# Kernel optimization log

Hardware: AMD Instinct MI355X
Metric: run time of the kernel (lower is better)

## Reference

```python
import jax, jax.numpy as jnp
import numpy as np

N, E, K, H, F_IN, F_OUT, Q = 50000, 1600000, 4, 4, 32, 32, 1


def setup_inputs() -> dict:
    key = jax.random.key(0)
    ks = jax.random.split(key, 5)
    x = jax.random.normal(ks[0], (N, H, F_IN, Q), dtype=jnp.float32)
    edge_index = jax.random.randint(ks[1], (2, E), 0, N, dtype=jnp.int64)
    edge_weight = jax.random.uniform(ks[2], (E,), dtype=jnp.float32)
    stdv = 1.0 / np.sqrt(F_IN * K)
    weight = jax.random.uniform(ks[3], (K, H, F_IN, F_OUT), dtype=jnp.float32, minval=-stdv, maxval=stdv)
    bias = jax.random.uniform(ks[4], (F_OUT,), dtype=jnp.float32, minval=-stdv, maxval=stdv)
    return {"x": x, "edge_index": edge_index, "edge_weight": edge_weight, "weight": weight, "bias": bias}


def reference(x, edge_index, edge_weight, weight, bias):
    # x: (n, h, f, q); weight: (K, h, f, g); edge_index: (2, E)
    n = x.shape[0]
    row, col = edge_index[0], edge_index[1]
    # remove_self_loops: zero out self-loop edges (static shapes, same math)
    mask = row != col
    ew = jnp.where(mask, edge_weight, jnp.zeros((), x.dtype))
    deg = jax.ops.segment_sum(mask.astype(x.dtype), row, num_segments=n)
    dinv = jnp.where(deg > 0, deg ** -0.5, jnp.zeros((), x.dtype))
    lap = -dinv[row] * ew * dinv[col]  # (E,)

    def spmm(t):
        # out[row] += lap * t[col]; t: (n, h, f, q)
        return jax.ops.segment_sum(lap[:, None, None, None] * t[col], row, num_segments=n)

    Kk = weight.shape[0]
    Tx0 = x
    out = jnp.einsum('nhfq,hfg->ngq', Tx0, weight[0])
    Tx1 = spmm(Tx0)
    out = out + jnp.einsum('nhfq,hfg->ngq', Tx1, weight[1])
    for k in range(2, Kk):
        Tx2 = 2.0 * spmm(Tx1) - Tx0
        out = out + jnp.einsum('nhfq,hfg->ngq', Tx2, weight[k])
        Tx0, Tx1 = Tx1, Tx2
    out = out[:, None]  # (n, 1, g, q) per collapse_H unsqueeze
    out = out + bias.reshape(1, 1, -1, 1)
    return out
```

## Files before the change

### kernel.cpp

```cpp
#include <hip/hip_runtime.h>


#define FEAT 128
#define GOUT 32
#define NCH 4
#define CHF 32
#define SCB 256
#define CH 4096
#define WCAP 16384
#define CAP 12032
#define TROW 160
#define UNR 8

typedef unsigned int uint;
typedef unsigned short ushort;

__device__ __forceinline__ ushort f2bf(float f) {
    uint u = __float_as_uint(f);
    return (ushort)((u + 0x7fffu + ((u >> 16) & 1u)) >> 16);
}
__device__ __forceinline__ float bflo(uint u) { return __uint_as_float(u << 16); }
__device__ __forceinline__ float bfhi(uint u) { return __uint_as_float(u & 0xffff0000u); }
__device__ __forceinline__ int tidx(int i) { return i + ((i >> 4) << 2); }

__global__ __launch_bounds__(1024) void bin_kernel(
    const int* __restrict__ ei, const float* __restrict__ ew, int E,
    int* __restrict__ bucketCursor, uint2* __restrict__ staging) {
    __shared__ int hist[256];
    __shared__ int base[256];
    int e0 = blockIdx.x * CH;
    int e1 = min(e0 + CH, E);
    int t = threadIdx.x;
    if (t < 256) hist[t] = 0;
    __syncthreads();
    for (int e = e0 + t; e < e1; e += 1024) {
        int r = ei[e], c = ei[(size_t)E + e];
        if (r != c) atomicAdd(&hist[r >> 8], 1);
    }
    __syncthreads();
    if (t < 256) {
        int h = hist[t];
        if (h > 0) {
            int run = atomicAdd(&bucketCursor[t], h);
            base[t] = t * CAP + run;
        }
        hist[t] = 0;
    }
    __syncthreads();
    for (int e = e0 + t; e < e1; e += 1024) {
        int r = ei[e], c = ei[(size_t)E + e];
        if (r == c) continue;
        float w = ew[e];
        int bk = r >> 8;
        int j = atomicAdd(&hist[bk], 1);
        int idx = base[bk] + j;
        if (idx < (bk + 1) * CAP)
            staging[idx] = make_uint2(__float_as_uint(w), ((uint)c << 16) | (uint)(r & 255));
    }
}

__global__ __launch_bounds__(256) void bucket_count_kernel(
    const uint2* __restrict__ staging, const int* __restrict__ bucketCursor,
    int* __restrict__ cnt, int n) {
    __shared__ int hist[256];
    int b = blockIdx.x;
    int t = threadIdx.x;
    hist[t] = 0;
    __syncthreads();
    int nrec = bucketCursor[b];
    const uint2* src = staging + (size_t)b * CAP;
    for (int k = t; k < nrec; k += 256)
        atomicAdd(&hist[src[k].y & 255], 1);
    __syncthreads();
    int r = (b << 8) + t;
    if (r < n) cnt[r] = hist[t];
}

__global__ void scan1_kernel(const int* __restrict__ cnt, int* __restrict__ partial,
                             int* __restrict__ blockSums, float* __restrict__ dinv, int n) {
    __shared__ int buf[2][SCB];
    int t = threadIdx.x;
    int i = blockIdx.x * SCB + t;
    int v = (i < n) ? cnt[i] : 0;
    if (i < n) dinv[i] = (v > 0) ? rsqrtf((float)v) : 0.0f;
    buf[0][t] = v;
    __syncthreads();
    int src = 0;
    for (int off = 1; off < SCB; off <<= 1) {
        int d = src ^ 1;
        buf[d][t] = buf[src][t] + ((t >= off) ? buf[src][t - off] : 0);
        __syncthreads();
        src = d;
    }
    int incl = buf[src][t];
    if (i < n) partial[i] = incl - v;
    if (t == SCB - 1) blockSums[blockIdx.x] = incl;
}

__global__ void scan2_kernel(const int* __restrict__ blockSums, int* __restrict__ blockOffsets,
                             int nb, int* __restrict__ total_out) {
    __shared__ int buf[2][SCB];
    __shared__ int carry_s;
    if (threadIdx.x == 0) carry_s = 0;
    __syncthreads();
    for (int base = 0; base < nb; base += SCB) {
        int i = base + (int)threadIdx.x;
        int v = (i < nb) ? blockSums[i] : 0;
        buf[0][threadIdx.x] = v;
        __syncthreads();
        int src = 0;
        for (int off = 1; off < SCB; off <<= 1) {
            int d = src ^ 1;
            buf[d][threadIdx.x] = buf[src][threadIdx.x] +
                                  ((threadIdx.x >= (unsigned)off) ? buf[src][threadIdx.x - off] : 0);
            __syncthreads();
            src = d;
        }
        int incl = buf[src][threadIdx.x];
        int c = carry_s;
        if (i < nb) blockOffsets[i] = c + incl - v;
        __syncthreads();
        if (threadIdx.x == SCB - 1) carry_s = c + incl;
        __syncthreads();
    }
    if (threadIdx.x == 0) *total_out = carry_s;
}

__global__ void scan3_kernel(const int* __restrict__ partial, const int* __restrict__ blockOffsets,
                             int* __restrict__ offsets, int n) {
    int i = blockIdx.x * blockDim.x + threadIdx.x;
    if (i < n) offsets[i] = partial[i] + blockOffsets[i / SCB];
}

__global__ __launch_bounds__(256) void scatter_kernel(
    const uint2* __restrict__ staging, const int* __restrict__ bucketCursor,
    const int* __restrict__ offsets, const float* __restrict__ dinv,
    uint* __restrict__ csr, int n) {
    __shared__ uint win[WCAP];
    __shared__ int roff[256];
    __shared__ int rcur[256];
    __shared__ float dloc[256];
    int b = blockIdx.x;
    int r0 = b << 8;
    int nrows = min(256, n - r0);
    int t = threadIdx.x;
    if (t < nrows) {
        roff[t] = offsets[r0 + t];
        dloc[t] = dinv[r0 + t];
    }
    rcur[t] = 0;
    __syncthreads();
    int wbeg = roff[0];
    int nrec = bucketCursor[b];
    bool fit = (nrec <= WCAP);
    const uint2* src = staging + (size_t)b * CAP;
    for (int k = t; k < nrec; k += 256) {
        uint2 rec = src[k];
        int col = rec.y >> 16;
        int rl = rec.y & 255;
        float lap = -dloc[rl] * __uint_as_float(rec.x) * dinv[col];
        uint colap = ((uint)col << 16) | (uint)f2bf(lap);
        int pos = roff[rl] + atomicAdd(&rcur[rl], 1);
        if (fit) win[pos - wbeg] = colap;
        else csr[pos] = colap;
    }
    __syncthreads();
    if (fit)
        for (int k = t; k < nrec; k += 256) csr[wbeg + k] = win[k];
}

__global__ __launch_bounds__(256) void cvt_einsum0_kernel(
    const float* __restrict__ x, ushort* __restrict__ xb,
    const float* __restrict__ W0, const float* __restrict__ bias,
    float* __restrict__ out, int n) {
    __shared__ __align__(16) float4 sW4[FEAT * GOUT / 4];
    __shared__ __align__(16) float sT[8 * TROW];
    const float* sW = (const float*)sW4;
    int t = threadIdx.x;
    const float4* wsrc = (const float4*)W0;
    for (int idx = t; idx < FEAT * GOUT / 4; idx += 256) sW4[idx] = wsrc[idx];
    int node = blockIdx.x * 8 + (t >> 5);
    int f0 = 4 * (t & 31);
    float4 v = make_float4(0.f, 0.f, 0.f, 0.f);
    if (node < n) {
        v = *(const float4*)(x + (size_t)node * FEAT + f0);
        ushort4 o;
        o.x = f2bf(v.x); o.y = f2bf(v.y); o.z = f2bf(v.z); o.w = f2bf(v.w);
        int j0 = f0 >> 5;
        *(ushort4*)(xb + ((size_t)j0 * n + node) * CHF + (f0 & 31)) = o;
    }
    int nl = t >> 5;
    *(float4*)&sT[nl * TROW + tidx(f0)] = v;
    __syncthreads();
    int l32 = t & 31;
    int q = l32 & 7;
    int part = l32 >> 3;
    float4 a4 = make_float4(0.f, 0.f, 0.f, 0.f);
#pragma unroll
    for (int j = 0; j < 8; ++j) {
        float4 t4 = *(const float4*)&sT[nl * TROW + tidx(part * 32 + 4 * j)];
        const float* wv0 = &sW[(part * 32 + 4 * j) * GOUT + 4 * q];
        float4 w0 = *(const float4*)(wv0);
        float4 w1 = *(const float4*)(wv0 + GOUT);
        float4 w2 = *(const float4*)(wv0 + 2 * GOUT);
        float4 w3 = *(const float4*)(wv0 + 3 * GOUT);
        a4.x += t4.x * w0.x + t4.y * w1.x + t4.z * w2.x + t4.w * w3.x;
        a4.y += t4.x * w0.y + t4.y * w1.y + t4.z * w2.y + t4.w * w3.y;
        a4.z += t4.x * w0.z + t4.y * w1.z + t4.z * w2.z + t4.w * w3.z;
        a4.w += t4.x * w0.w + t4.y * w1.w + t4.z * w2.w + t4.w * w3.w;
    }
    a4.x += __shfl_down(a4.x, 8);  a4.y += __shfl_down(a4.y, 8);
    a4.z += __shfl_down(a4.z, 8);  a4.w += __shfl_down(a4.w, 8);
    a4.x += __shfl_down(a4.x, 16); a4.y += __shfl_down(a4.y, 16);
    a4.z += __shfl_down(a4.z, 16); a4.w += __shfl_down(a4.w, 16);
    if (part == 0 && node < n) {
        const float4 b4 = *(const float4*)(bias + 4 * q);
        float4 r;
        r.x = a4.x + b4.x; r.y = a4.y + b4.y; r.z = a4.z + b4.z; r.w = a4.w + b4.w;
        *(float4*)(out + (size_t)node * GOUT + 4 * q) = r;
    }
}

__global__ __launch_bounds__(512) void spmm_chunk_kernel(
    const ushort* __restrict__ inb, const ushort* __restrict__ sub,
    ushort* __restrict__ outb, const int* __restrict__ offsets,
    const uint* __restrict__ csr, const float* __restrict__ Wk,
    float* __restrict__ out, int n, int has_sub, int nbj) {
    __shared__ __align__(16) float sW[CHF * GOUT];
    __shared__ float sT2[8][8][CHF + 1];
    int j = blockIdx.x / nbj;
    int b = blockIdx.x % nbj;
    int t = threadIdx.x;
    const float4* wsrc = (const float4*)(Wk + j * CHF * GOUT);
    for (int i2 = t; i2 < CHF * GOUT / 4; i2 += 512) ((float4*)sW)[i2] = wsrc[i2];
    int w = t >> 6, lane = t & 63, s = lane >> 3, u = lane & 7;
    int node = b * 64 + w * 8 + s;
    int beg = 0, deg = 0;
    if (node < n) { beg = offsets[node]; deg = offsets[node + 1] - beg; }
    int m = deg;
    m = max(m, __shfl_xor(m, 8));
    m = max(m, __shfl_xor(m, 16));
    m = max(m, __shfl_xor(m, 32));
    const uint2* inb_u2 = (const uint2*)inb;
    size_t jb2 = (size_t)j * n * 8;
    size_t obase = jb2 + (size_t)node * 8 + u;
    uint2 sv = make_uint2(0u, 0u);
    if (has_sub && node < n) sv = ((const uint2*)sub)[obase];
    float a0 = 0.f, a1 = 0.f, a2 = 0.f, a3 = 0.f;
    for (int it = 0; it < m; it += UNR) {
        uint q[UNR];
        uint2 uu[UNR];
#pragma unroll
        for (int k = 0; k < UNR; ++k) {
            int idx = it + k;
            q[k] = (idx < deg) ? csr[beg + idx] : 0u;
        }
#pragma unroll
        for (int k = 0; k < UNR; ++k)
            uu[k] = inb_u2[jb2 + (size_t)(q[k] >> 16) * 8 + u];
#pragma unroll
        for (int k = 0; k < UNR; ++k) {
            float l = bflo(q[k]);
            a0 += l * bflo(uu[k].x);
            a1 += l * bfhi(uu[k].x);
            a2 += l * bflo(uu[k].y);
            a3 += l * bfhi(uu[k].y);
        }
    }
    if (has_sub) {
        a0 = 2.f * a0 - bflo(sv.x);
        a1 = 2.f * a1 - bfhi(sv.x);
        a2 = 2.f * a2 - bflo(sv.y);
        a3 = 2.f * a3 - bfhi(sv.y);
    }
    if (node < n) {
        uint2 o;
        o.x = (uint)f2bf(a0) | ((uint)f2bf(a1) << 16);
        o.y = (uint)f2bf(a2) | ((uint)f2bf(a3) << 16);
        ((uint2*)outb)[obase] = o;
    }
    sT2[w][s][4 * u + 0] = a0;
    sT2[w][s][4 * u + 1] = a1;
    sT2[w][s][4 * u + 2] = a2;
    sT2[w][s][4 * u + 3] = a3;
    __syncthreads();
    float e0 = 0.f, e1 = 0.f, e2 = 0.f, e3 = 0.f;
#pragma unroll
    for (int i = 0; i < CHF; ++i) {
        float tv = sT2[w][s][i];
        e0 += tv * sW[i * GOUT + u];
        e1 += tv * sW[i * GOUT + u + 8];
        e2 += tv * sW[i * GOUT + u + 16];
        e3 += tv * sW[i * GOUT + u + 24];
    }
    if (node < n) {
        float* po = out + (size_t)node * GOUT;
        atomicAdd(po + u, e0);
        atomicAdd(po + u + 8, e1);
        atomicAdd(po + u + 16, e2);
        atomicAdd(po + u + 24, e3);
    }
}

extern "C" void kernel_launch(void* const* d_in, const int* in_sizes, int n_in,
                              void* d_out, int out_size, void* d_ws, size_t ws_size,
                              hipStream_t stream) {
    const float* x = (const float*)d_in[0];
    const int* ei = (const int*)d_in[1];
    const float* ew = (const float*)d_in[2];
    const float* W = (const float*)d_in[3];
    const float* bias = (const float*)d_in[4];
    float* out = (float*)d_out;

    const int N = in_sizes[0] / FEAT;
    const int E = in_sizes[1] / 2;
    const int NB = (N + SCB - 1) / SCB;
    const int NBUK = (N + 255) >> 8;
    const int NBJ = (((N + 63) / 64 + 7) / 8) * 8;

    char* p = (char*)d_ws;
    auto alloc = [&](size_t bytes) {
        char* q = p;
        p += (bytes + 255) & ~(size_t)255;
        return q;
    };
    int* cnt = (int*)alloc((size_t)N * 4);
    int* offsets = (int*)alloc(((size_t)N + 1) * 4);
    float* dinv = (float*)alloc((size_t)N * 4);
    int* partial = (int*)alloc((size_t)N * 4);
    int* blockSums = (int*)alloc((size_t)NB * 4);
    int* blockOffsets = (int*)alloc((size_t)NB * 4);
    int* bucketCursor = (int*)alloc((size_t)NBUK * 4);
    uint* csr = (uint*)alloc(((size_t)E + 64) * 4);
    ushort* xb = (ushort*)alloc((size_t)N * FEAT * 2);
    ushort* Ab = (ushort*)alloc((size_t)N * FEAT * 2);
    ushort* Bb = (ushort*)alloc((size_t)N * FEAT * 2);
    uint2* staging = (uint2*)Ab;
    (void)ws_size;

    hipMemsetAsync(bucketCursor, 0, (size_t)NBUK * 4, stream);

    bin_kernel<<<(E + CH - 1) / CH, 1024, 0, stream>>>(ei, ew, E, bucketCursor, staging);
    bucket_count_kernel<<<NBUK, 256, 0, stream>>>(staging, bucketCursor, cnt, N);
    scan1_kernel<<<NB, SCB, 0, stream>>>(cnt, partial, blockSums, dinv, N);
    scan2_kernel<<<1, SCB, 0, stream>>>(blockSums, blockOffsets, NB, offsets + N);
    scan3_kernel<<<NB, SCB, 0, stream>>>(partial, blockOffsets, offsets, N);
    scatter_kernel<<<NBUK, 256, 0, stream>>>(staging, bucketCursor, offsets, dinv, csr, N);

    cvt_einsum0_kernel<<<(N + 7) / 8, 256, 0, stream>>>(x, xb, W, bias, out, N);

    dim3 sg(NCH * NBJ);
    spmm_chunk_kernel<<<sg, 512, 0, stream>>>(xb, nullptr, Ab, offsets, csr,
                                              W + 1 * FEAT * GOUT, out, N, 0, NBJ);
    spmm_chunk_kernel<<<sg, 512, 0, stream>>>(Ab, xb, Bb, offsets, csr,
                                              W + 2 * FEAT * GOUT, out, N, 1, NBJ);
    spmm_chunk_kernel<<<sg, 512, 0, stream>>>(Bb, Ab, Ab, offsets, csr,
                                              W + 3 * FEAT * GOUT, out, N, 1, NBJ);
}
```

Before: 357.8 us.

## Sort nodes by degree so SpMM waves process similar-length rows

Result: slower. 470.9 us (+31.6%).

```diff
diff --git a/kernel.cpp b/kernel.cpp
--- a/kernel.cpp
+++ b/kernel.cpp
@@ -132,6 +132,45 @@
     if (i < n) offsets[i] = partial[i] + blockOffsets[i / SCB];
 }
 
+__global__ __launch_bounds__(256) void deg_hist_kernel(
+    const int* __restrict__ cnt, int* __restrict__ dhist, int n) {
+    __shared__ int h[256];
+    int t = threadIdx.x;
+    h[t] = 0;
+    __syncthreads();
+    int i = blockIdx.x * 256 + t;
+    if (i < n) atomicAdd(&h[min(cnt[i], 255)], 1);
+    __syncthreads();
+    if (h[t] > 0) atomicAdd(&dhist[t], h[t]);
+}
+
+__global__ __launch_bounds__(256) void deg_scan_kernel(
+    const int* __restrict__ dhist, int* __restrict__ dbase) {
+    __shared__ int buf[2][256];
+    int t = threadIdx.x;
+    int v = dhist[t];
+    buf[0][t] = v;
+    __syncthreads();
+    int src = 0;
+    for (int off = 1; off < 256; off <<= 1) {
+        int d = src ^ 1;
+        buf[d][t] = buf[src][t] + ((t >= off) ? buf[src][t - off] : 0);
+        __syncthreads();
+        src = d;
+    }
+    dbase[t] = buf[src][t] - v;
+}
+
+__global__ __launch_bounds__(256) void deg_scatter_kernel(
+    const int* __restrict__ cnt, const int* __restrict__ dbase,
+    int* __restrict__ dcur, int* __restrict__ perm, int n) {
+    int i = blockIdx.x * 256 + threadIdx.x;
+    if (i >= n) return;
+    int d = min(cnt[i], 255);
+    int pos = dbase[d] + atomicAdd(&dcur[d], 1);
+    perm[pos] = i;
+}
+
 __global__ __launch_bounds__(256) void scatter_kernel(
     const uint2* __restrict__ staging, const int* __restrict__ bucketCursor,
     const int* __restrict__ offsets, const float* __restrict__ dinv,
@@ -224,7 +263,8 @@
 __global__ __launch_bounds__(512) void spmm_chunk_kernel(
     const ushort* __restrict__ inb, const ushort* __restrict__ sub,
     ushort* __restrict__ outb, const int* __restrict__ offsets,
-    const uint* __restrict__ csr, const float* __restrict__ Wk,
+    const uint* __restrict__ csr, const int* __restrict__ perm,
+    const float* __restrict__ Wk,
     float* __restrict__ out, int n, int has_sub, int nbj) {
     __shared__ __align__(16) float sW[CHF * GOUT];
     __shared__ float sT2[8][8][CHF + 1];
@@ -234,7 +274,8 @@
     const float4* wsrc = (const float4*)(Wk + j * CHF * GOUT);
     for (int i2 = t; i2 < CHF * GOUT / 4; i2 += 512) ((float4*)sW)[i2] = wsrc[i2];
     int w = t >> 6, lane = t & 63, s = lane >> 3, u = lane & 7;
-    int node = b * 64 + w * 8 + s;
+    int idx0 = b * 64 + w * 8 + s;
+    int node = (idx0 < n) ? perm[idx0] : n;
     int beg = 0, deg = 0;
     if (node < n) { beg = offsets[node]; deg = offsets[node + 1] - beg; }
     int m = deg;
@@ -331,6 +372,10 @@
     int* blockSums = (int*)alloc((size_t)NB * 4);
     int* blockOffsets = (int*)alloc((size_t)NB * 4);
     int* bucketCursor = (int*)alloc((size_t)NBUK * 4);
+    int* dhist = (int*)alloc(512 * 4);
+    int* dcur = dhist + 256;
+    int* dbase = (int*)alloc(256 * 4);
+    int* perm = (int*)alloc((size_t)N * 4);
     uint* csr = (uint*)alloc(((size_t)E + 64) * 4);
     ushort* xb = (ushort*)alloc((size_t)N * FEAT * 2);
     ushort* Ab = (ushort*)alloc((size_t)N * FEAT * 2);
@@ -339,21 +384,25 @@
     (void)ws_size;
 
     hipMemsetAsync(bucketCursor, 0, (size_t)NBUK * 4, stream);
+    hipMemsetAsync(dhist, 0, 512 * 4, stream);
 
     bin_kernel<<<(E + CH - 1) / CH, 1024, 0, stream>>>(ei, ew, E, bucketCursor, staging);
     bucket_count_kernel<<<NBUK, 256, 0, stream>>>(staging, bucketCursor, cnt, N);
     scan1_kernel<<<NB, SCB, 0, stream>>>(cnt, partial, blockSums, dinv, N);
     scan2_kernel<<<1, SCB, 0, stream>>>(blockSums, blockOffsets, NB, offsets + N);
     scan3_kernel<<<NB, SCB, 0, stream>>>(partial, blockOffsets, offsets, N);
+    deg_hist_kernel<<<NBUK, 256, 0, stream>>>(cnt, dhist, N);
+    deg_scan_kernel<<<1, 256, 0, stream>>>(dhist, dbase);
+    deg_scatter_kernel<<<NBUK, 256, 0, stream>>>(cnt, dbase, dcur, perm, N);
     scatter_kernel<<<NBUK, 256, 0, stream>>>(staging, bucketCursor, offsets, dinv, csr, N);
 
     cvt_einsum0_kernel<<<(N + 7) / 8, 256, 0, stream>>>(x, xb, W, bias, out, N);
 
     dim3 sg(NCH * NBJ);
-    spmm_chunk_kernel<<<sg, 512, 0, stream>>>(xb, nullptr, Ab, offsets, csr,
+    spmm_chunk_kernel<<<sg, 512, 0, stream>>>(xb, nullptr, Ab, offsets, csr, perm,
                                               W + 1 * FEAT * GOUT, out, N, 0, NBJ);
-    spmm_chunk_kernel<<<sg, 512, 0, stream>>>(Ab, xb, Bb, offsets, csr,
+    spmm_chunk_kernel<<<sg, 512, 0, stream>>>(Ab, xb, Bb, offsets, csr, perm,
                                               W + 2 * FEAT * GOUT, out, N, 1, NBJ);
-    spmm_chunk_kernel<<<sg, 512, 0, stream>>>(Bb, Ab, Ab, offsets, csr,
+    spmm_chunk_kernel<<<sg, 512, 0, stream>>>(Bb, Ab, Ab, offsets, csr, perm,
                                               W + 3 * FEAT * GOUT, out, N, 1, NBJ);
 }
```
